# Kernel tuning notes

Hardware: AMD Instinct MI355X
Metric: run time of the kernel (lower is better)

## Reference

```python
import jax, jax.numpy as jnp
import numpy as np

N, E, F_IN, HID, OUT, HEADS, NG = 40000, 640000, 64, 128, 64, 4, 64
EPS = 1e-5

def setup_inputs() -> dict:
    key = jax.random.key(0)
    ks = jax.random.split(key, 32)
    d = {}
    d['x'] = jax.random.normal(ks[0], (N, F_IN), dtype=jnp.float32)
    d['edge_index'] = jax.random.randint(ks[1], (2, E), 0, N, dtype=jnp.int64)
    d['batch'] = jnp.sort(jax.random.randint(ks[2], (N,), 0, NG, dtype=jnp.int64))
    fins = [F_IN, HID, HID]
    for i in range(3):
        kk = jax.random.split(ks[3 + i], 6)
        fin = fins[i]
        d[f'W{i}'] = jax.random.normal(kk[0], (fin, HEADS * HID), dtype=jnp.float32) / np.sqrt(fin)
        d[f'as{i}'] = jax.random.normal(kk[1], (HEADS, HID), dtype=jnp.float32) / np.sqrt(HID)
        d[f'ad{i}'] = jax.random.normal(kk[2], (HEADS, HID), dtype=jnp.float32) / np.sqrt(HID)
        d[f'b{i}'] = jnp.zeros((HID,), dtype=jnp.float32)
        d[f'g{i}'] = jnp.ones((HID,), dtype=jnp.float32) + 0.05 * jax.random.normal(kk[3], (HID,), dtype=jnp.float32)
        d[f'be{i}'] = 0.05 * jax.random.normal(kk[4], (HID,), dtype=jnp.float32)
    d['fc1_w'] = jax.random.normal(ks[10], (HID, HID), dtype=jnp.float32) / np.sqrt(HID)
    d['fc1_b'] = jnp.zeros((HID,), dtype=jnp.float32)
    d['fc2_w'] = jax.random.normal(ks[11], (HID, OUT), dtype=jnp.float32) / np.sqrt(HID)
    d['fc2_b'] = jnp.zeros((OUT,), dtype=jnp.float32)
    return d

def _gat(x, src, dst, W, a_s, a_d, b):
    # PyG GATConv, heads=4, concat=False (mean over heads)
    xh = (x @ W).reshape(N, HEADS, HID)            # [N,H,C]
    s_src = jnp.einsum('nhc,hc->nh', xh, a_s)      # [N,H]
    s_dst = jnp.einsum('nhc,hc->nh', xh, a_d)
    e = jax.nn.leaky_relu(s_src[src] + s_dst[dst], 0.2)   # [Etot,H]
    m = jax.ops.segment_max(e, dst, num_segments=N)
    p = jnp.exp(e - m[dst])
    denom = jax.ops.segment_sum(p, dst, num_segments=N)
    alpha = p / denom[dst]                          # segment softmax over dst
    msg = xh[src] * alpha[:, :, None]               # [Etot,H,C]
    out = jax.ops.segment_sum(msg, dst, num_segments=N)  # [N,H,C]
    return out.mean(axis=1) + b

def _bn_eval(x, g, be):
    # running_mean=0, running_var=1 (eval mode)
    return x * (g / jnp.sqrt(1.0 + EPS)) + be

def reference(x, edge_index, batch, W0, as0, ad0, b0, g0, be0, W1, as1, ad1, b1, g1, be1, W2, as2, ad2, b2, g2, be2, fc1_w, fc1_b, fc2_w, fc2_b):
    loop = jnp.arange(N, dtype=edge_index.dtype)
    src = jnp.concatenate([edge_index[0], loop])   # add_self_loops (PyG default)
    dst = jnp.concatenate([edge_index[1], loop])
    h = x
    params = [(W0, as0, ad0, b0, g0, be0), (W1, as1, ad1, b1, g1, be1), (W2, as2, ad2, b2, g2, be2)]
    for (W, a_s, a_d, b, g, be) in params:
        h = _gat(h, src, dst, W, a_s, a_d, b)
        h = jax.nn.relu(_bn_eval(h, g, be))
        # dropout is identity in eval mode
    sums = jax.ops.segment_sum(h, batch, num_segments=NG)
    cnt = jax.ops.segment_sum(jnp.ones((N,), h.dtype), batch, num_segments=NG)
    pooled = sums / jnp.maximum(cnt, 1.0)[:, None]   # global_mean_pool [NG,HID]
    out = jax.nn.relu(pooled @ fc1_w + fc1_b)
    return out @ fc2_w + fc2_b
```

## Files before the change

kernel.cpp:

```cpp
#include <hip/hip_runtime.h>
#include <hip/hip_fp16.h>
#include <math.h>

#define N_NODES 40000
#define N_EDGES 640000
#define FIN 64
#define HID 128
#define OUTDIM 64
#define HEADS 4
#define NGROUPS 64
#define NCOLS 512

typedef _Float16 half8 __attribute__((ext_vector_type(8)));
typedef float f32x4 __attribute__((ext_vector_type(4)));

__device__ __forceinline__ float lrelu(float x) { return x > 0.f ? x : 0.2f * x; }

__device__ __forceinline__ void wave_lds_fence() {
    asm volatile("s_waitcnt lgkmcnt(0)" ::: "memory");
}

#define PREP_X4   (N_NODES * FIN / 4)
#define PREP_WSWZ 20480
#define PREP_V    2560
__global__ void prep_kernel(const float* __restrict__ x, __half* __restrict__ x16,
                            const float* __restrict__ W0, const float* __restrict__ W1,
                            const float* __restrict__ W2,
                            _Float16* __restrict__ F0, _Float16* __restrict__ F1,
                            _Float16* __restrict__ F2,
                            const float* __restrict__ as0, const float* __restrict__ ad0,
                            const float* __restrict__ as1, const float* __restrict__ ad1,
                            const float* __restrict__ as2, const float* __restrict__ ad2,
                            float* __restrict__ v0, float* __restrict__ v1,
                            float* __restrict__ v2) {
    int id = blockIdx.x * 256 + threadIdx.x;
    if (id < PREP_X4) {
        int i4 = id * 4;
        float4 v = *(const float4*)(x + i4);
        __half2 a = __floats2half2_rn(v.x, v.y);
        __half2 b = __floats2half2_rn(v.z, v.w);
        *(__half2*)(x16 + i4)     = a;
        *(__half2*)(x16 + i4 + 2) = b;
        return;
    }
    id -= PREP_X4;
    if (id < PREP_WSWZ) {
        const float* W; _Float16* F; int Kin;
        if (id < 4096)       { W = W0; F = F0; Kin = FIN; }
        else if (id < 12288) { W = W1; F = F1; Kin = HID; id -= 4096; }
        else                 { W = W2; F = F2; Kin = HID; id -= 12288; }
        int KP = Kin * 4;
        int NKg = KP / 32;
        int lane = id & 63;
        int blob = id >> 6;
        int k0g = blob % NKg;
        int cb  = blob / NKg;
        int col = cb * 16 + (lane & 15);
        int kkb = k0g * 32 + (lane >> 4) * 8;
        half8 v;
        #pragma unroll
        for (int e = 0; e < 8; ++e) {
            int kk = kkb + e;
            int k = kk & (Kin - 1);
            int h = kk / Kin;
            v[e] = (_Float16)(0.25f * W[(size_t)k * NCOLS + h * HID + col]);
        }
        *(half8*)(F + (size_t)blob * 512 + lane * 8) = v;
        return;
    }
    id -= PREP_WSWZ;
    if (id < PREP_V) {
        const float* W; const float* as_; const float* ad_; float* v; int j = id;
        if (j < FIN * 8)              { W = W0; as_ = as0; ad_ = ad0; v = v0; }
        else if (j < (FIN + HID) * 8) { W = W1; as_ = as1; ad_ = ad1; v = v1; j -= FIN * 8; }
        else                          { W = W2; as_ = as2; ad_ = ad2; v = v2; j -= (FIN + HID) * 8; }
        int k = j >> 3, sd = (j >> 2) & 1, h = j & 3;
        const float* av = sd ? ad_ : as_;
        float acc = 0.f;
        for (int c = 0; c < HID; ++c)
            acc += W[(size_t)k * NCOLS + h * HID + c] * av[h * HID + c];
        v[k * 8 + sd * 4 + h] = acc;
    }
}

__global__ void deg_count_kernel(const int* __restrict__ ei, int* deg) {
    int e = blockIdx.x * blockDim.x + threadIdx.x;
    if (e < N_EDGES) atomicAdd(&deg[ei[N_EDGES + e]], 1);
}

__global__ void scan1_kernel(const int* __restrict__ deg, int* offsets, int* partial) {
    __shared__ int buf[256];
    int t = threadIdx.x;
    int i = blockIdx.x * 256 + t;
    int v = (i < N_NODES) ? deg[i] + 1 : 0;
    buf[t] = v;
    __syncthreads();
    for (int off = 1; off < 256; off <<= 1) {
        int y = (t >= off) ? buf[t - off] : 0;
        __syncthreads();
        buf[t] += y;
        __syncthreads();
    }
    if (i < N_NODES) offsets[i] = buf[t] - v;
    if (t == 255) partial[blockIdx.x] = buf[255];
}

__global__ void scan2_kernel(int* partial, int nb) {
    __shared__ int buf[256];
    int t = threadIdx.x;
    int v = (t < nb) ? partial[t] : 0;
    buf[t] = v;
    __syncthreads();
    for (int off = 1; off < 256; off <<= 1) {
        int y = (t >= off) ? buf[t - off] : 0;
        __syncthreads();
        buf[t] += y;
        __syncthreads();
    }
    if (t < nb) partial[t] = buf[t] - v;
}

__global__ void scan3_kernel(int* offsets, int* pos, const int* __restrict__ partial) {
    int i = blockIdx.x * 256 + threadIdx.x;
    if (i < N_NODES) {
        int o = offsets[i] + partial[i >> 8];
        offsets[i] = o;
        pos[i] = o;
    }
    if (i == 0) offsets[N_NODES] = N_EDGES + N_NODES;
}

__global__ void scatter_kernel(const int* __restrict__ ei, int* pos, int* csr_src) {
    int i = blockIdx.x * blockDim.x + threadIdx.x;
    if (i < N_EDGES) {
        int s = ei[i];
        int d = ei[N_EDGES + i];
        csr_src[atomicAdd(&pos[d], 1)] = s;
    } else if (i < N_EDGES + N_NODES) {
        int nn = i - N_EDGES;
        csr_src[atomicAdd(&pos[nn], 1)] = nn;
    }
}

template <int K>
__global__ __launch_bounds__(256) void scores3_kernel(const __half* __restrict__ x,
                                                      const float* __restrict__ v,
                                                      float* __restrict__ ssrc,
                                                      float* __restrict__ sdst) {
    __shared__ float vs[K * 8];
    int t = threadIdx.x;
    for (int i = t; i < K * 8; i += 256) vs[i] = v[i];
    __syncthreads();
    int node = blockIdx.x * 256 + t;
    if (node >= N_NODES) return;
    const __half* xr = x + (size_t)node * K;
    f32x4 as = {0.f, 0.f, 0.f, 0.f};
    f32x4 ad = {0.f, 0.f, 0.f, 0.f};
    #pragma unroll 4
    for (int k0 = 0; k0 < K; k0 += 8) {
        uint4 u = *(const uint4*)(xr + k0);
        __half2* hp = (__half2*)&u;
        #pragma unroll
        for (int q = 0; q < 4; ++q) {
            float2 f = __half22float2(hp[q]);
            int k = k0 + 2 * q;
            as += f.x * *(const f32x4*)&vs[k * 8];
            ad += f.x * *(const f32x4*)&vs[k * 8 + 4];
            as += f.y * *(const f32x4*)&vs[(k + 1) * 8];
            ad += f.y * *(const f32x4*)&vs[(k + 1) * 8 + 4];
        }
    }
    *(f32x4*)(ssrc + node * 4) = as;
    *(f32x4*)(sdst + node * 4) = ad;
}

template <int K, bool SCORES>
__global__ __launch_bounds__(512) void fused_layer_kernel(
        const __half* __restrict__ tab16,
        const float* __restrict__ s_src,
        const float* __restrict__ s_dst,
        const int* __restrict__ offsets,
        const int* __restrict__ csr_src,
        const _Float16* __restrict__ Wf,
        const float* __restrict__ bias,
        const float* __restrict__ gamma,
        const float* __restrict__ beta,
        const float* __restrict__ vtab_next,
        __half* __restrict__ h16out,
        float* __restrict__ ssrc_o,
        float* __restrict__ sdst_o) {
    constexpr int KP = 4 * K;
    constexpr int EPR = (K == 128) ? 4 : 8;
    constexpr int LPE = 64 / EPR;
    constexpr int NKg = KP / 32;

    __shared__ _Float16 As[32][KP + 8];
    __shared__ __align__(16) char uali[11520];
    __shared__ float bn_s[3][HID];
    __shared__ float vs[SCORES ? HID * 8 : 8];

    int (*roff)[72]    = (int(*)[72])uali;
    float (*al)[72][4] = (float(*)[72][4])(uali + 8 * 72 * 4);
    _Float16 (*tb)[136] = (_Float16(*)[136])uali;

    int t = threadIdx.x;
    int lane = t & 63;
    int wv = t >> 6;
    int bm = blockIdx.x * 32;

    if (t < HID) {
        bn_s[0][t] = bias[t];
        bn_s[1][t] = gamma[t] * rsqrtf(1.f + 1e-5f);
        bn_s[2][t] = beta[t];
    }
    if (SCORES)
        for (int i = t; i < HID * 8; i += 512) vs[i] = vtab_next[i];

    int cgrp = lane & (LPE - 1);
    int egoff = lane / LPE;
    const char* xb = (const char*)tab16 + cgrp * 16;

    if (lane < 8) {
        roff[wv][64 + lane] = 0;
        *(f32x4*)&al[wv][64 + lane][0] = f32x4{0.f, 0.f, 0.f, 0.f};
    }

    for (int i = 0; i < 4; ++i) {
        int nl = wv * 4 + i;
        int n = bm + nl;
        int start = offsets[n], end = offsets[n + 1];
        int deg = end - start;
        const float4 sd = *(const float4*)(s_dst + n * 4);
        float acc[4][8] = {};

        if (deg <= 64) {
            bool act = lane < deg;
            int src = act ? csr_src[start + lane] : 0;
            float4 ss = *(const float4*)(s_src + src * 4);
            float e0 = act ? lrelu(ss.x + sd.x) : -1e30f;
            float e1 = act ? lrelu(ss.y + sd.y) : -1e30f;
            float e2 = act ? lrelu(ss.z + sd.z) : -1e30f;
            float e3 = act ? lrelu(ss.w + sd.w) : -1e30f;
            float m0 = e0, m1 = e1, m2 = e2, m3 = e3;
            #pragma unroll
            for (int o = 32; o > 0; o >>= 1) {
                m0 = fmaxf(m0, __shfl_xor(m0, o));
                m1 = fmaxf(m1, __shfl_xor(m1, o));
                m2 = fmaxf(m2, __shfl_xor(m2, o));
                m3 = fmaxf(m3, __shfl_xor(m3, o));
            }
            float p0 = __expf(e0 - m0), p1 = __expf(e1 - m1);
            float p2 = __expf(e2 - m2), p3 = __expf(e3 - m3);
            float s0 = p0, s1 = p1, s2 = p2, s3 = p3;
            #pragma unroll
            for (int o = 32; o > 0; o >>= 1) {
                s0 += __shfl_xor(s0, o);
                s1 += __shfl_xor(s1, o);
                s2 += __shfl_xor(s2, o);
                s3 += __shfl_xor(s3, o);
            }
            f32x4 av = {p0 / s0, p1 / s1, p2 / s2, p3 / s3};
            roff[wv][lane] = src * (K * 2);
            *(f32x4*)&al[wv][lane][0] = av;
            wave_lds_fence();

            for (int j = 0; j < deg; j += EPR) {
                int eg = j + egoff;
                f32x4 a4 = *(const f32x4*)&al[wv][eg][0];
                uint4 u = *(const uint4*)(xb + roff[wv][eg]);
                __half2* hp = (__half2*)&u;
                #pragma unroll
                for (int q = 0; q < 4; ++q) {
                    float2 f = __half22float2(hp[q]);
                    #pragma unroll
                    for (int h = 0; h < 4; ++h) {
                        acc[h][2 * q]     += a4[h] * f.x;
                        acc[h][2 * q + 1] += a4[h] * f.y;
                    }
                }
            }
        } else {
            float m0 = -1e30f, m1 = -1e30f, m2 = -1e30f, m3 = -1e30f;
            for (int j0 = 0; j0 < deg; j0 += 64) {
                int j = j0 + lane;
                bool act = j < deg;
                int src = act ? csr_src[start + j] : 0;
                float4 ss = *(const float4*)(s_src + src * 4);
                m0 = fmaxf(m0, act ? lrelu(ss.x + sd.x) : -1e30f);
                m1 = fmaxf(m1, act ? lrelu(ss.y + sd.y) : -1e30f);
                m2 = fmaxf(m2, act ? lrelu(ss.z + sd.z) : -1e30f);
                m3 = fmaxf(m3, act ? lrelu(ss.w + sd.w) : -1e30f);
            }
            #pragma unroll
            for (int o = 32; o > 0; o >>= 1) {
                m0 = fmaxf(m0, __shfl_xor(m0, o));
                m1 = fmaxf(m1, __shfl_xor(m1, o));
                m2 = fmaxf(m2, __shfl_xor(m2, o));
                m3 = fmaxf(m3, __shfl_xor(m3, o));
            }
            float s0 = 0.f, s1 = 0.f, s2 = 0.f, s3 = 0.f;
            for (int j0 = 0; j0 < deg; j0 += 64) {
                int j = j0 + lane;
                bool act = j < deg;
                int src = act ? csr_src[start + j] : 0;
                float4 ss = *(const float4*)(s_src + src * 4);
                s0 += act ? __expf(lrelu(ss.x + sd.x) - m0) : 0.f;
                s1 += act ? __expf(lrelu(ss.y + sd.y) - m1) : 0.f;
                s2 += act ? __expf(lrelu(ss.z + sd.z) - m2) : 0.f;
                s3 += act ? __expf(lrelu(ss.w + sd.w) - m3) : 0.f;
            }
            #pragma unroll
            for (int o = 32; o > 0; o >>= 1) {
                s0 += __shfl_xor(s0, o);
                s1 += __shfl_xor(s1, o);
                s2 += __shfl_xor(s2, o);
                s3 += __shfl_xor(s3, o);
            }
            float i0 = 1.f / s0, i1 = 1.f / s1, i2 = 1.f / s2, i3 = 1.f / s3;
            for (int j0 = 0; j0 < deg; j0 += 64) {
                int j = j0 + lane;
                bool act = j < deg;
                int src = act ? csr_src[start + j] : 0;
                float4 ss = *(const float4*)(s_src + src * 4);
                f32x4 av;
                av[0] = act ? __expf(lrelu(ss.x + sd.x) - m0) * i0 : 0.f;
                av[1] = act ? __expf(lrelu(ss.y + sd.y) - m1) * i1 : 0.f;
                av[2] = act ? __expf(lrelu(ss.z + sd.z) - m2) * i2 : 0.f;
                av[3] = act ? __expf(lrelu(ss.w + sd.w) - m3) * i3 : 0.f;
                roff[wv][lane] = act ? src * (K * 2) : 0;
                *(f32x4*)&al[wv][lane][0] = av;
                wave_lds_fence();
                int cend = min(64, deg - j0);
                for (int j2 = 0; j2 < cend; j2 += EPR) {
                    int eg = j2 + egoff;
                    f32x4 a4 = *(const f32x4*)&al[wv][eg][0];
                    uint4 u = *(const uint4*)(xb + roff[wv][eg]);
                    __half2* hp = (__half2*)&u;
                    #pragma unroll
                    for (int q = 0; q < 4; ++q) {
                        float2 f = __half22float2(hp[q]);
                        #pragma unroll
                        for (int h = 0; h < 4; ++h) {
                            acc[h][2 * q]     += a4[h] * f.x;
                            acc[h][2 * q + 1] += a4[h] * f.y;
                        }
                    }
                }
                wave_lds_fence();
            }
        }

        #pragma unroll
        for (int stride = LPE; stride < 64; stride <<= 1) {
            #pragma unroll
            for (int h = 0; h < 4; ++h)
                #pragma unroll
                for (int r = 0; r < 8; ++r)
                    acc[h][r] += __shfl_xor(acc[h][r], stride);
        }
        if (lane < LPE) {
            #pragma unroll
            for (int h = 0; h < 4; ++h) {
                half8 v;
                #pragma unroll
                for (int r = 0; r < 8; ++r) v[r] = (_Float16)acc[h][r];
                *(half8*)&As[nl][h * K + cgrp * 8] = v;
            }
        }
        wave_lds_fence();
    }
    __syncthreads();

    int wm = wv >> 2, wn = wv & 3;
    int lr = lane & 15;
    int lk = (lane >> 4) * 8;
    int lg = lane >> 4;
    f32x4 acc2[2] = {};
    #pragma unroll
    for (int k0g = 0; k0g < NKg; ++k0g) {
        half8 af = *(const half8*)&As[wm * 16 + lr][k0g * 32 + lk];
        #pragma unroll
        for (int nn = 0; nn < 2; ++nn) {
            int cb = wn * 2 + nn;
            half8 bf = *(const half8*)(Wf + ((size_t)(cb * NKg + k0g) << 9) + lane * 8);
            acc2[nn] = __builtin_amdgcn_mfma_f32_16x16x32_f16(af, bf, acc2[nn], 0, 0, 0);
        }
    }

    #pragma unroll
    for (int nn = 0; nn < 2; ++nn) {
        int col = wn * 32 + nn * 16 + lr;
        float b = bn_s[0][col], g = bn_s[1][col], be = bn_s[2][col];
        #pragma unroll
        for (int r = 0; r < 4; ++r) {
            float o = acc2[nn][r] + b;
            o = o * g + be;
            tb[wm * 16 + lg * 4 + r][col] = (_Float16)fmaxf(o, 0.f);
        }
    }
    __syncthreads();

    {
        int row = t >> 4;
        int c0 = (t & 15) * 8;
        half8 v0 = *(const half8*)&tb[row][c0];
        *(half8*)((_Float16*)h16out + (size_t)(bm + row) * HID + c0) = v0;
    }

    if (SCORES) {
        if (t < 256) {
            int node = t >> 3, j = t & 7;
            float sacc = 0.f;
            #pragma unroll 2
            for (int k0 = 0; k0 < HID; k0 += 8) {
                half8 hv = *(const half8*)&tb[node][k0];
                #pragma unroll
                for (int e = 0; e < 8; ++e)
                    sacc += (float)hv[e] * vs[(k0 + e) * 8 + j];
            }
            if (j < 4) ssrc_o[(bm + node) * 4 + j] = sacc;
            else       sdst_o[(bm + node) * 4 + (j - 4)] = sacc;
        }
    }
}

__global__ __launch_bounds__(128) void pool_kernel(const __half* __restrict__ h,
                                                   const int* __restrict__ batch,
                                                   float* pooled, float* counts) {
    int t = threadIdx.x;
    int which = t >> 6;
    int c2 = (t & 63) * 2;
    int n0 = blockIdx.x * 256 + which;
    int n1 = min(blockIdx.x * 256 + 256, N_NODES);
    if (n0 >= N_NODES) return;
    int cg = batch[n0];
    float a0 = 0.f, a1 = 0.f, cnt = 0.f;
    for (int n = n0; n < n1; n += 2) {
        int g = batch[n];
        if (g != cg) {
            atomicAdd(&pooled[cg * HID + c2], a0);
            atomicAdd(&pooled[cg * HID + c2 + 1], a1);
            if ((t & 63) == 0) atomicAdd(&counts[cg], cnt);
            a0 = 0.f; a1 = 0.f; cnt = 0.f; cg = g;
        }
        uint u = *(const uint*)(h + (size_t)n * HID + c2);
        __half2 hh = *(__half2*)&u;
        float2 f = __half22float2(hh);
        a0 += f.x; a1 += f.y; cnt += 1.f;
    }
    atomicAdd(&pooled[cg * HID + c2], a0);
    atomicAdd(&pooled[cg * HID + c2 + 1], a1);
    if ((t & 63) == 0) atomicAdd(&counts[cg], cnt);
}

__global__ __launch_bounds__(128) void head_kernel(const float* __restrict__ pooled,
                                                   const float* __restrict__ counts,
                                                   const float* __restrict__ fc1_w,
                                                   const float* __restrict__ fc1_b,
                                                   const float* __restrict__ fc2_w,
                                                   const float* __restrict__ fc2_b,
                                                   float* __restrict__ out) {
    int gI = blockIdx.x;
    int t = threadIdx.x;
    __shared__ float p[HID], hb[HID];
    p[t] = pooled[gI * HID + t] / fmaxf(counts[gI], 1.f);
    __syncthreads();
    float a = fc1_b[t];
    #pragma unroll 4
    for (int k = 0; k < HID; ++k) a += p[k] * fc1_w[k * HID + t];
    hb[t] = fmaxf(a, 0.f);
    __syncthreads();
    if (t < OUTDIM) {
        float o = fc2_b[t];
        #pragma unroll 4
        for (int k = 0; k < HID; ++k) o += hb[k] * fc2_w[k * OUTDIM + t];
        out[gI * OUTDIM + t] = o;
    }
}

extern "C" void kernel_launch(void* const* d_in, const int* in_sizes, int n_in,
                              void* d_out, int out_size, void* d_ws, size_t ws_size,
                              hipStream_t stream) {
    const float* x     = (const float*)d_in[0];
    const int*   ei    = (const int*)d_in[1];
    const int*   batch = (const int*)d_in[2];
    const float* W[3]  = {(const float*)d_in[3],  (const float*)d_in[9],  (const float*)d_in[15]};
    const float* As_[3] = {(const float*)d_in[4],  (const float*)d_in[10], (const float*)d_in[16]};
    const float* Ad[3] = {(const float*)d_in[5],  (const float*)d_in[11], (const float*)d_in[17]};
    const float* Bb[3] = {(const float*)d_in[6],  (const float*)d_in[12], (const float*)d_in[18]};
    const float* Gg[3] = {(const float*)d_in[7],  (const float*)d_in[13], (const float*)d_in[19]};
    const float* Be[3] = {(const float*)d_in[8],  (const float*)d_in[14], (const float*)d_in[20]};
    const float* fc1_w = (const float*)d_in[21];
    const float* fc1_b = (const float*)d_in[22];
    const float* fc2_w = (const float*)d_in[23];
    const float* fc2_b = (const float*)d_in[24];

    char* ws = (char*)d_ws;
    size_t off = 0;
    auto alloc = [&](size_t bytes) {
        void* p = ws + off;
        off = (off + bytes + 255) & ~(size_t)255;
        return p;
    };
    __half* x16    = (__half*)alloc((size_t)N_NODES * FIN * 2);
    __half* h16A   = (__half*)alloc((size_t)N_NODES * HID * 2);
    __half* h16B   = (__half*)alloc((size_t)N_NODES * HID * 2);
    _Float16* Wf[3];
    Wf[0] = (_Float16*)alloc((size_t)(4 * FIN) * HID * 2);
    Wf[1] = (_Float16*)alloc((size_t)(4 * HID) * HID * 2);
    Wf[2] = (_Float16*)alloc((size_t)(4 * HID) * HID * 2);
    float* vtab[3];
    vtab[0] = (float*)alloc((size_t)FIN * 8 * 4);
    vtab[1] = (float*)alloc((size_t)HID * 8 * 4);
    vtab[2] = (float*)alloc((size_t)HID * 8 * 4);
    float* ssrcA   = (float*)alloc((size_t)N_NODES * HEADS * 4);
    float* sdstA   = (float*)alloc((size_t)N_NODES * HEADS * 4);
    float* ssrcB   = (float*)alloc((size_t)N_NODES * HEADS * 4);
    float* sdstB   = (float*)alloc((size_t)N_NODES * HEADS * 4);
    int*   deg     = (int*)alloc((size_t)N_NODES * 4);
    int*   offsets = (int*)alloc((size_t)(N_NODES + 1) * 4);
    int*   pos     = (int*)alloc((size_t)N_NODES * 4);
    int*   partial = (int*)alloc((size_t)256 * 4);
    int*   csr     = (int*)alloc((size_t)(N_EDGES + N_NODES) * 4);
    float* pooled  = (float*)alloc((size_t)NGROUPS * HID * 4 + (size_t)NGROUPS * 4);
    float* counts  = pooled + (size_t)NGROUPS * HID;

    const int PREP_TOTAL = PREP_X4 + PREP_WSWZ + PREP_V;
    prep_kernel<<<(PREP_TOTAL + 255) / 256, 256, 0, stream>>>(
        x, x16, W[0], W[1], W[2], Wf[0], Wf[1], Wf[2],
        As_[0], Ad[0], As_[1], Ad[1], As_[2], Ad[2], vtab[0], vtab[1], vtab[2]);

    const int NB = (N_NODES + 255) / 256;
    hipMemsetAsync(deg, 0, (size_t)N_NODES * 4, stream);
    deg_count_kernel<<<(N_EDGES + 255) / 256, 256, 0, stream>>>(ei, deg);
    scan1_kernel<<<NB, 256, 0, stream>>>(deg, offsets, partial);
    scan2_kernel<<<1, 256, 0, stream>>>(partial, NB);
    scan3_kernel<<<NB, 256, 0, stream>>>(offsets, pos, partial);
    scatter_kernel<<<(N_EDGES + N_NODES + 255) / 256, 256, 0, stream>>>(ei, pos, csr);

    scores3_kernel<64><<<NB, 256, 0, stream>>>(x16, vtab[0], ssrcA, sdstA);

    fused_layer_kernel<64, true><<<N_NODES / 32, 512, 0, stream>>>(
        x16, ssrcA, sdstA, offsets, csr, Wf[0], Bb[0], Gg[0], Be[0],
        vtab[1], h16A, ssrcB, sdstB);
    fused_layer_kernel<128, true><<<N_NODES / 32, 512, 0, stream>>>(
        h16A, ssrcB, sdstB, offsets, csr, Wf[1], Bb[1], Gg[1], Be[1],
        vtab[2], h16B, ssrcA, sdstA);
    fused_layer_kernel<128, false><<<N_NODES / 32, 512, 0, stream>>>(
        h16B, ssrcA, sdstA, offsets, csr, Wf[2], Bb[2], Gg[2], Be[2],
        nullptr, h16A, nullptr, nullptr);

    hipMemsetAsync(pooled, 0, (size_t)NGROUPS * HID * 4 + (size_t)NGROUPS * 4, stream);
    pool_kernel<<<(N_NODES + 255) / 256, 128, 0, stream>>>(h16A, batch, pooled, counts);
    head_kernel<<<NGROUPS, 128, 0, stream>>>(pooled, counts, fc1_w, fc1_b, fc2_w, fc2_b,
                                             (float*)d_out);
}
```

Before: 394.0 us.

## Precompute edge softmax weights in a separate edge kernel with atomic denominators

Moves the per-edge attention softmax out of the fused aggregation kernel into a new edge-parallel kernel. That kernel writes exp(leaky_relu(score)) per edge and head to a buffer and atomically accumulates per-destination denominators. The fused layer kernel then only normalizes and gathers, which drops the wave-level max/sum reductions, the LDS staging and the high-degree fallback path. The cost is about 10 MB of extra edge-value traffic per layer, many float atomics, a csr_dst array, and removal of max subtraction, so large scores could overflow exp.

Result: slower. 828.3 us (+110.2%).

```diff
diff --git a/kernel.cpp b/kernel.cpp
--- a/kernel.cpp
+++ b/kernel.cpp
@@ -15,10 +15,6 @@
 typedef float f32x4 __attribute__((ext_vector_type(4)));
 
 __device__ __forceinline__ float lrelu(float x) { return x > 0.f ? x : 0.2f * x; }
-
-__device__ __forceinline__ void wave_lds_fence() {
-    asm volatile("s_waitcnt lgkmcnt(0)" ::: "memory");
-}
 
 #define PREP_X4   (N_NODES * FIN / 4)
 #define PREP_WSWZ 20480
@@ -130,15 +126,20 @@
     if (i == 0) offsets[N_NODES] = N_EDGES + N_NODES;
 }
 
-__global__ void scatter_kernel(const int* __restrict__ ei, int* pos, int* csr_src) {
+__global__ void scatter_kernel(const int* __restrict__ ei, int* pos,
+                               int* csr_src, int* csr_dst) {
     int i = blockIdx.x * blockDim.x + threadIdx.x;
     if (i < N_EDGES) {
         int s = ei[i];
         int d = ei[N_EDGES + i];
-        csr_src[atomicAdd(&pos[d], 1)] = s;
+        int p = atomicAdd(&pos[d], 1);
+        csr_src[p] = s;
+        csr_dst[p] = d;
     } else if (i < N_EDGES + N_NODES) {
         int nn = i - N_EDGES;
-        csr_src[atomicAdd(&pos[nn], 1)] = nn;
+        int p = atomicAdd(&pos[nn], 1);
+        csr_src[p] = nn;
+        csr_dst[p] = nn;
     }
 }
 
@@ -174,11 +175,34 @@
     *(f32x4*)(sdst + node * 4) = ad;
 }
 
+__global__ __launch_bounds__(256) void edge_alpha_kernel(const float* __restrict__ ssrc,
+                                                         const float* __restrict__ sdst,
+                                                         const int* __restrict__ csr_src,
+                                                         const int* __restrict__ csr_dst,
+                                                         float* __restrict__ val,
+                                                         float* __restrict__ denom) {
+    int j = blockIdx.x * 256 + threadIdx.x;
+    if (j >= N_EDGES + N_NODES) return;
+    int s = csr_src[j], d = csr_dst[j];
+    float4 a = *(const float4*)(ssrc + s * 4);
+    float4 b = *(const float4*)(sdst + d * 4);
+    float4 v;
+    v.x = __expf(lrelu(a.x + b.x));
+    v.y = __expf(lrelu(a.y + b.y));
+    v.z = __expf(lrelu(a.z + b.z));
+    v.w = __expf(lrelu(a.w + b.w));
+    *(float4*)(val + (size_t)j * 4) = v;
+    atomicAdd(&denom[d * 4 + 0], v.x);
+    atomicAdd(&denom[d * 4 + 1], v.y);
+    atomicAdd(&denom[d * 4 + 2], v.z);
+    atomicAdd(&denom[d * 4 + 3], v.w);
+}
+
 template <int K, bool SCORES>
 __global__ __launch_bounds__(512) void fused_layer_kernel(
         const __half* __restrict__ tab16,
-        const float* __restrict__ s_src,
-        const float* __restrict__ s_dst,
+        const float* __restrict__ val,
+        const float* __restrict__ denom,
         const int* __restrict__ offsets,
         const int* __restrict__ csr_src,
         const _Float16* __restrict__ Wf,
@@ -195,13 +219,9 @@
     constexpr int NKg = KP / 32;
 
     __shared__ _Float16 As[32][KP + 8];
-    __shared__ __align__(16) char uali[11520];
+    __shared__ _Float16 tb[32][136];
     __shared__ float bn_s[3][HID];
     __shared__ float vs[SCORES ? HID * 8 : 8];
-
-    int (*roff)[72]    = (int(*)[72])uali;
-    float (*al)[72][4] = (float(*)[72][4])(uali + 8 * 72 * 4);
-    _Float16 (*tb)[136] = (_Float16(*)[136])uali;
 
     int t = threadIdx.x;
     int lane = t & 63;
@@ -219,134 +239,37 @@
     int cgrp = lane & (LPE - 1);
     int egoff = lane / LPE;
     const char* xb = (const char*)tab16 + cgrp * 16;
-
-    if (lane < 8) {
-        roff[wv][64 + lane] = 0;
-        *(f32x4*)&al[wv][64 + lane][0] = f32x4{0.f, 0.f, 0.f, 0.f};
-    }
 
     for (int i = 0; i < 4; ++i) {
         int nl = wv * 4 + i;
         int n = bm + nl;
         int start = offsets[n], end = offsets[n + 1];
         int deg = end - start;
-        const float4 sd = *(const float4*)(s_dst + n * 4);
+        float4 dn = *(const float4*)(denom + n * 4);
+        f32x4 inv = {1.f / dn.x, 1.f / dn.y, 1.f / dn.z, 1.f / dn.w};
         float acc[4][8] = {};
 
-        if (deg <= 64) {
-            bool act = lane < deg;
-            int src = act ? csr_src[start + lane] : 0;
-            float4 ss = *(const float4*)(s_src + src * 4);
-            float e0 = act ? lrelu(ss.x + sd.x) : -1e30f;
-            float e1 = act ? lrelu(ss.y + sd.y) : -1e30f;
-            float e2 = act ? lrelu(ss.z + sd.z) : -1e30f;
-            float e3 = act ? lrelu(ss.w + sd.w) : -1e30f;
-            float m0 = e0, m1 = e1, m2 = e2, m3 = e3;
+        for (int j = 0; j < deg; j += EPR) {
+            int eg = j + egoff;
+            bool act = eg < deg;
+            int ec = act ? eg : deg - 1;
+            int src = csr_src[start + ec];
+            float4 vv = *(const float4*)(val + (size_t)(start + ec) * 4);
+            f32x4 a4;
+            a4[0] = act ? vv.x * inv[0] : 0.f;
+            a4[1] = act ? vv.y * inv[1] : 0.f;
+            a4[2] = act ? vv.z * inv[2] : 0.f;
+            a4[3] = act ? vv.w * inv[3] : 0.f;
+            uint4 u = *(const uint4*)(xb + (uint)src * (K * 2));
+            __half2* hp = (__half2*)&u;
             #pragma unroll
-            for (int o = 32; o > 0; o >>= 1) {
-                m0 = fmaxf(m0, __shfl_xor(m0, o));
-                m1 = fmaxf(m1, __shfl_xor(m1, o));
-                m2 = fmaxf(m2, __shfl_xor(m2, o));
-                m3 = fmaxf(m3, __shfl_xor(m3, o));
-            }
-            float p0 = __expf(e0 - m0), p1 = __expf(e1 - m1);
-            float p2 = __expf(e2 - m2), p3 = __expf(e3 - m3);
-            float s0 = p0, s1 = p1, s2 = p2, s3 = p3;
-            #pragma unroll
-            for (int o = 32; o > 0; o >>= 1) {
-                s0 += __shfl_xor(s0, o);
-                s1 += __shfl_xor(s1, o);
-                s2 += __shfl_xor(s2, o);
-                s3 += __shfl_xor(s3, o);
-            }
-            f32x4 av = {p0 / s0, p1 / s1, p2 / s2, p3 / s3};
-            roff[wv][lane] = src * (K * 2);
-            *(f32x4*)&al[wv][lane][0] = av;
-            wave_lds_fence();
-
-            for (int j = 0; j < deg; j += EPR) {
-                int eg = j + egoff;
-                f32x4 a4 = *(const f32x4*)&al[wv][eg][0];
-                uint4 u = *(const uint4*)(xb + roff[wv][eg]);
-                __half2* hp = (__half2*)&u;
+            for (int q = 0; q < 4; ++q) {
+                float2 f = __half22float2(hp[q]);
                 #pragma unroll
-                for (int q = 0; q < 4; ++q) {
-                    float2 f = __half22float2(hp[q]);
-                    #pragma unroll
-                    for (int h = 0; h < 4; ++h) {
-                        acc[h][2 * q]     += a4[h] * f.x;
-                        acc[h][2 * q + 1] += a4[h] * f.y;
-                    }
+                for (int h = 0; h < 4; ++h) {
+                    acc[h][2 * q]     += a4[h] * f.x;
+                    acc[h][2 * q + 1] += a4[h] * f.y;
                 }
-            }
-        } else {
-            float m0 = -1e30f, m1 = -1e30f, m2 = -1e30f, m3 = -1e30f;
-            for (int j0 = 0; j0 < deg; j0 += 64) {
-                int j = j0 + lane;
-                bool act = j < deg;
-                int src = act ? csr_src[start + j] : 0;
-                float4 ss = *(const float4*)(s_src + src * 4);
-                m0 = fmaxf(m0, act ? lrelu(ss.x + sd.x) : -1e30f);
-                m1 = fmaxf(m1, act ? lrelu(ss.y + sd.y) : -1e30f);
-                m2 = fmaxf(m2, act ? lrelu(ss.z + sd.z) : -1e30f);
-                m3 = fmaxf(m3, act ? lrelu(ss.w + sd.w) : -1e30f);
-            }
-            #pragma unroll
-            for (int o = 32; o > 0; o >>= 1) {
-                m0 = fmaxf(m0, __shfl_xor(m0, o));
-                m1 = fmaxf(m1, __shfl_xor(m1, o));
-                m2 = fmaxf(m2, __shfl_xor(m2, o));
-                m3 = fmaxf(m3, __shfl_xor(m3, o));
-            }
-            float s0 = 0.f, s1 = 0.f, s2 = 0.f, s3 = 0.f;
-            for (int j0 = 0; j0 < deg; j0 += 64) {
-                int j = j0 + lane;
-                bool act = j < deg;
-                int src = act ? csr_src[start + j] : 0;
-                float4 ss = *(const float4*)(s_src + src * 4);
-                s0 += act ? __expf(lrelu(ss.x + sd.x) - m0) : 0.f;
-                s1 += act ? __expf(lrelu(ss.y + sd.y) - m1) : 0.f;
-                s2 += act ? __expf(lrelu(ss.z + sd.z) - m2) : 0.f;
-                s3 += act ? __expf(lrelu(ss.w + sd.w) - m3) : 0.f;
-            }
-            #pragma unroll
-            for (int o = 32; o > 0; o >>= 1) {
-                s0 += __shfl_xor(s0, o);
-                s1 += __shfl_xor(s1, o);
-                s2 += __shfl_xor(s2, o);
-                s3 += __shfl_xor(s3, o);
-            }
-            float i0 = 1.f / s0, i1 = 1.f / s1, i2 = 1.f / s2, i3 = 1.f / s3;
-            for (int j0 = 0; j0 < deg; j0 += 64) {
-                int j = j0 + lane;
-                bool act = j < deg;
-                int src = act ? csr_src[start + j] : 0;
-                float4 ss = *(const float4*)(s_src + src * 4);
-                f32x4 av;
-                av[0] = act ? __expf(lrelu(ss.x + sd.x) - m0) * i0 : 0.f;
-                av[1] = act ? __expf(lrelu(ss.y + sd.y) - m1) * i1 : 0.f;
-                av[2] = act ? __expf(lrelu(ss.z + sd.z) - m2) * i2 : 0.f;
-                av[3] = act ? __expf(lrelu(ss.w + sd.w) - m3) * i3 : 0.f;
-                roff[wv][lane] = act ? src * (K * 2) : 0;
-                *(f32x4*)&al[wv][lane][0] = av;
-                wave_lds_fence();
-                int cend = min(64, deg - j0);
-                for (int j2 = 0; j2 < cend; j2 += EPR) {
-                    int eg = j2 + egoff;
-                    f32x4 a4 = *(const f32x4*)&al[wv][eg][0];
-                    uint4 u = *(const uint4*)(xb + roff[wv][eg]);
-                    __half2* hp = (__half2*)&u;
-                    #pragma unroll
-                    for (int q = 0; q < 4; ++q) {
-                        float2 f = __half22float2(hp[q]);
-                        #pragma unroll
-                        for (int h = 0; h < 4; ++h) {
-                            acc[h][2 * q]     += a4[h] * f.x;
-                            acc[h][2 * q + 1] += a4[h] * f.y;
-                        }
-                    }
-                }
-                wave_lds_fence();
             }
         }
 
@@ -367,7 +290,6 @@
                 *(half8*)&As[nl][h * K + cgrp * 8] = v;
             }
         }
-        wave_lds_fence();
     }
     __syncthreads();
 
@@ -517,11 +439,14 @@
     float* sdstA   = (float*)alloc((size_t)N_NODES * HEADS * 4);
     float* ssrcB   = (float*)alloc((size_t)N_NODES * HEADS * 4);
     float* sdstB   = (float*)alloc((size_t)N_NODES * HEADS * 4);
+    float* val     = (float*)alloc((size_t)(N_EDGES + N_NODES) * 4 * 4);
+    float* denoms  = (float*)alloc((size_t)3 * N_NODES * 4 * 4);
     int*   deg     = (int*)alloc((size_t)N_NODES * 4);
     int*   offsets = (int*)alloc((size_t)(N_NODES + 1) * 4);
     int*   pos     = (int*)alloc((size_t)N_NODES * 4);
     int*   partial = (int*)alloc((size_t)256 * 4);
     int*   csr     = (int*)alloc((size_t)(N_EDGES + N_NODES) * 4);
+    int*   csrd    = (int*)alloc((size_t)(N_EDGES + N_NODES) * 4);
     float* pooled  = (float*)alloc((size_t)NGROUPS * HID * 4 + (size_t)NGROUPS * 4);
     float* counts  = pooled + (size_t)NGROUPS * HID;
 
@@ -532,22 +457,31 @@
 
     const int NB = (N_NODES + 255) / 256;
     hipMemsetAsync(deg, 0, (size_t)N_NODES * 4, stream);
+    hipMemsetAsync(denoms, 0, (size_t)3 * N_NODES * 4 * 4, stream);
     deg_count_kernel<<<(N_EDGES + 255) / 256, 256, 0, stream>>>(ei, deg);
     scan1_kernel<<<NB, 256, 0, stream>>>(deg, offsets, partial);
     scan2_kernel<<<1, 256, 0, stream>>>(partial, NB);
     scan3_kernel<<<NB, 256, 0, stream>>>(offsets, pos, partial);
-    scatter_kernel<<<(N_EDGES + N_NODES + 255) / 256, 256, 0, stream>>>(ei, pos, csr);
+    scatter_kernel<<<(N_EDGES + N_NODES + 255) / 256, 256, 0, stream>>>(ei, pos, csr, csrd);
+
+    const int EB = (N_EDGES + N_NODES + 255) / 256;
+    float* den0 = denoms;
+    float* den1 = denoms + (size_t)N_NODES * 4;
+    float* den2 = denoms + (size_t)2 * N_NODES * 4;
 
     scores3_kernel<64><<<NB, 256, 0, stream>>>(x16, vtab[0], ssrcA, sdstA);
 
+    edge_alpha_kernel<<<EB, 256, 0, stream>>>(ssrcA, sdstA, csr, csrd, val, den0);
     fused_layer_kernel<64, true><<<N_NODES / 32, 512, 0, stream>>>(
-        x16, ssrcA, sdstA, offsets, csr, Wf[0], Bb[0], Gg[0], Be[0],
+        x16, val, den0, offsets, csr, Wf[0], Bb[0], Gg[0], Be[0],
         vtab[1], h16A, ssrcB, sdstB);
+    edge_alpha_kernel<<<EB, 256, 0, stream>>>(ssrcB, sdstB, csr, csrd, val, den1);
     fused_layer_kernel<128, true><<<N_NODES / 32, 512, 0, stream>>>(
-        h16A, ssrcB, sdstB, offsets, csr, Wf[1], Bb[1], Gg[1], Be[1],
+        h16A, val, den1, offsets, csr, Wf[1], Bb[1], Gg[1], Be[1],
         vtab[2], h16B, ssrcA, sdstA);
+    edge_alpha_kernel<<<EB, 256, 0, stream>>>(ssrcA, sdstA, csr, csrd, val, den2);
     fused_layer_kernel<128, false><<<N_NODES / 32, 512, 0, stream>>>(
-        h16B, ssrcA, sdstA, offsets, csr, Wf[2], Bb[2], Gg[2], Be[2],
+        h16B, val, den2, offsets, csr, Wf[2], Bb[2], Gg[2], Be[2],
         nullptr, h16A, nullptr, nullptr);
 
     hipMemsetAsync(pooled, 0, (size_t)NGROUPS * HID * 4 + (size_t)NGROUPS * 4, stream);
```
